# Kernel tuning notes

Measured on AMD Instinct MI355X. Metric: run time of the kernel, lower is better.

## Reference

```python
import jax, jax.numpy as jnp
import numpy as np

DIM = 512
HEADS = 8
RES = 14
HEAD_DIM = DIM // HEADS
N = RES * RES


def _make_bias_idxs(res):
    pts = [(i, j) for i in range(res) for j in range(res)]
    offs = {}
    idxs = []
    for p1 in pts:
        for p2 in pts:
            o = (abs(p1[0] - p2[0]), abs(p1[1] - p2[1]))
            if o not in offs:
                offs[o] = len(offs)
            idxs.append(offs[o])
    return np.asarray(idxs, dtype=np.int32).reshape(res * res, res * res), len(offs)


def setup_inputs() -> dict:
    key = jax.random.key(0)
    ks = jax.random.split(key, 6)
    idxs, n_off = _make_bias_idxs(RES)  # n_off == 196 for res=14
    B = 128
    return {
        "x": jax.random.normal(ks[0], (B, DIM, RES, RES), dtype=jnp.float32),
        "qkv_w": jax.random.normal(ks[1], (3 * DIM, DIM), dtype=jnp.float32) * 0.02,
        "qkv_b": jnp.zeros((3 * DIM,), dtype=jnp.float32),
        "proj_w": jax.random.normal(ks[2], (DIM, DIM), dtype=jnp.float32) * 0.02,
        "proj_b": jnp.zeros((DIM,), dtype=jnp.float32),
        "attention_biases": jax.random.normal(ks[3], (HEADS, n_off), dtype=jnp.float32) * 0.02,
        "bias_idxs": jnp.asarray(idxs),
    }


def reference(x, qkv_w, qkv_b, proj_w, proj_b, attention_biases, bias_idxs):
    B, C, H, W = x.shape
    scale = HEAD_DIM ** -0.5
    # 1x1 conv == channel-wise linear
    qkv = jnp.einsum("oc,bchw->bohw", qkv_w, x) + qkv_b[None, :, None, None]
    q, k, v = jnp.split(qkv, 3, axis=1)
    # [B, heads, head_dim, N]
    q = q.reshape(B, HEADS, HEAD_DIM, N)
    k = k.reshape(B, HEADS, HEAD_DIM, N)
    v = v.reshape(B, HEADS, HEAD_DIM, N)
    attn = jnp.einsum("bhdn,bhdm->bhnm", q, k) * scale  # [B,h,N,N]
    bias = attention_biases[:, bias_idxs]  # gather -> [h,N,N]
    attn = jax.nn.softmax(attn + bias[None], axis=-1)
    out = jnp.einsum("bhnm,bhdm->bhdn", attn, v).reshape(B, C, H, W)
    return jnp.einsum("oc,bchw->bohw", proj_w, out) + proj_b[None, :, None, None]
```

## Files before the change

kernel.cpp:

```cpp
#include <hip/hip_runtime.h>
#include <hip/hip_bf16.h>
#include <math.h>

#define B_     128
#define DIM_   512
#define HEADS_ 8
#define HD_    64
#define N_     196
#define NP_    224
#define NROW_  208
#define SCALE_ 0.125f
#define BSTRIDE (DIM_ * N_)
#define J_     (B_ * NP_)

typedef unsigned short u16;
typedef unsigned int   u32;
typedef __attribute__((ext_vector_type(8))) short bf16x8;
typedef __attribute__((ext_vector_type(4))) float f32x4;

__device__ __forceinline__ u16 f2bf(float f) {
    u32 u = __float_as_uint(f);
    return (u16)((u + 0x7fffu + ((u >> 16) & 1u)) >> 16);
}
__device__ __forceinline__ void gload_lds16(const u16* g, u16* l) {
    __builtin_amdgcn_global_load_lds(
        (const __attribute__((address_space(1))) void*)g,
        (__attribute__((address_space(3))) void*)l, 16, 0, 0);
}

__global__ __launch_bounds__(256) void cvt_bf2(
    const float* __restrict__ a, u16* __restrict__ da, int n4a,
    const float* __restrict__ b, u16* __restrict__ db, int n4b)
{
    const int i = blockIdx.x * 256 + threadIdx.x;
    const float* src = blockIdx.y ? b : a;
    u16* dst = blockIdx.y ? db : da;
    const int n4 = blockIdx.y ? n4b : n4a;
    if (i < n4) {
        const float4 v = reinterpret_cast<const float4*>(src)[i];
        uint2 o;
        o.x = (u32)f2bf(v.x) | ((u32)f2bf(v.y) << 16);
        o.y = (u32)f2bf(v.z) | ((u32)f2bf(v.w) << 16);
        reinterpret_cast<uint2*>(dst)[i] = o;
    }
}

__global__ __launch_bounds__(256) void cvt_xT(
    const float* __restrict__ x, u16* __restrict__ XT)
{
    __shared__ float tile[64][65];
    const int t = threadIdx.x;
    const int jj = t & 63, ii = t >> 6;
    const int ct = blockIdx.x, ntb = blockIdx.y, b = blockIdx.z;
    const float* xb = x + ((size_t)b * DIM_ + ct * 64) * N_;
    const int n0 = ntb * 64;
    #pragma unroll
    for (int s = 0; s < 16; ++s) {
        const int i = ii + s * 4;
        const int n = n0 + jj;
        tile[i][jj] = (n < N_) ? xb[(size_t)i * N_ + n] : 0.f;
    }
    __syncthreads();
    u16* ot = XT + (size_t)b * NP_ * DIM_ + ct * 64;
    #pragma unroll
    for (int s = 0; s < 16; ++s) {
        const int nn = n0 + ii + s * 4;
        if (nn < N_) ot[(size_t)nn * DIM_ + jj] = f2bf(tile[jj][ii + s * 4]);
    }
}

__global__ __launch_bounds__(256) void mk_eb(
    const float* __restrict__ biases, const int* __restrict__ bidx,
    float* __restrict__ EB)
{
    const int n = blockIdx.x, h = blockIdx.y;
    const int m = threadIdx.x;
    if (m < NP_) {
        float v = 0.f;
        if (n < N_ && m < N_) v = __expf(biases[h * N_ + bidx[n * N_ + m]]);
        EB[((size_t)h * NROW_ + n) * NP_ + m] = v;
    }
}

template<bool QKV>
__global__ __launch_bounds__(256) void gemm128(
    const u16* __restrict__ Bt, const u16* __restrict__ W,
    const float* __restrict__ bias,
    u16* __restrict__ o_q, u16* __restrict__ o_k, u16* __restrict__ o_v,
    float* __restrict__ o_f)
{
    __shared__ u16 As[2][128 * 32];
    __shared__ u16 Bs[2][128 * 32];
    const int t = threadIdx.x;
    const int wave = t >> 6, lane = t & 63;
    const int m16 = lane & 15, quad = lane >> 4;

    constexpr int MT  = QKV ? 12 : 4;
    constexpr int NWG = (J_ / 128) * MT;
    const int bid = blockIdx.x;
    const int swz = (bid & 7) * (NWG / 8) + (bid >> 3);
    const int mt = swz % MT;
    const int jt = swz / MT;
    const int m0 = mt * 128, j0 = jt * 128;
    const int wy = wave >> 1, wx = wave & 1;

    const int srow  = (lane >> 2);
    const int schnk = (lane & 3) ^ ((lane >> 3) & 3);
    const u16* gA = W  + (size_t)(m0 + wave * 32 + srow) * DIM_ + schnk * 8;
    const u16* gB = Bt + (size_t)(j0 + wave * 32 + srow) * DIM_ + schnk * 8;

    const int rcol = (quad ^ ((m16 >> 1) & 3)) * 8;

    f32x4 acc[4][4];
    const f32x4 z4 = {0.f, 0.f, 0.f, 0.f};
    #pragma unroll
    for (int fi = 0; fi < 4; ++fi)
        #pragma unroll
        for (int fj = 0; fj < 4; ++fj) acc[fi][fj] = z4;

    #pragma unroll
    for (int cc = 0; cc < 2; ++cc) {
        const int c = wave * 2 + cc;
        gload_lds16(gA + (size_t)(cc * 16) * DIM_, As[0] + c * 512);
        gload_lds16(gB + (size_t)(cc * 16) * DIM_, Bs[0] + c * 512);
    }
    #pragma unroll
    for (int kt = 0; kt < 16; ++kt) {
        const int cur = kt & 1;
        __syncthreads();
        if (kt < 15) {
            #pragma unroll
            for (int cc = 0; cc < 2; ++cc) {
                const int c = wave * 2 + cc;
                gload_lds16(gA + (size_t)(cc * 16) * DIM_ + (kt + 1) * 32, As[cur ^ 1] + c * 512);
                gload_lds16(gB + (size_t)(cc * 16) * DIM_ + (kt + 1) * 32, Bs[cur ^ 1] + c * 512);
            }
        }
        bf16x8 af[4], bf[4];
        #pragma unroll
        for (int fi = 0; fi < 4; ++fi)
            af[fi] = *reinterpret_cast<const bf16x8*>(As[cur] + (wy * 64 + fi * 16 + m16) * 32 + rcol);
        #pragma unroll
        for (int fj = 0; fj < 4; ++fj)
            bf[fj] = *reinterpret_cast<const bf16x8*>(Bs[cur] + (wx * 64 + fj * 16 + m16) * 32 + rcol);
        #pragma unroll
        for (int fi = 0; fi < 4; ++fi)
            #pragma unroll
            for (int fj = 0; fj < 4; ++fj)
                acc[fi][fj] = __builtin_amdgcn_mfma_f32_16x16x32_bf16(af[fi], bf[fj], acc[fi][fj], 0, 0, 0);
    }

    const int mbase = m0 + wy * 64;
    float bb[4][4];
    #pragma unroll
    for (int fi = 0; fi < 4; ++fi)
        #pragma unroll
        for (int r = 0; r < 4; ++r) bb[fi][r] = bias[mbase + fi * 16 + quad * 4 + r];

    if (QKV) {
        const int part = mbase >> 9;
        const int h = (mbase & 511) >> 6;
        #pragma unroll
        for (int fj = 0; fj < 4; ++fj) {
            const int j = j0 + wx * 64 + fj * 16 + m16;
            const u32 b = (u32)j / 224u;
            const int n = j - (int)b * 224;
            if (part < 2) {
                u16* base = (part == 0 ? o_q : o_k) + (((size_t)b * HEADS_ + h) * NP_ + n) * HD_;
                #pragma unroll
                for (int fi = 0; fi < 4; ++fi) {
                    const int d0 = fi * 16 + quad * 4;
                    uint2 pk;
                    pk.x = (u32)f2bf(acc[fi][fj][0] + bb[fi][0]) | ((u32)f2bf(acc[fi][fj][1] + bb[fi][1]) << 16);
                    pk.y = (u32)f2bf(acc[fi][fj][2] + bb[fi][2]) | ((u32)f2bf(acc[fi][fj][3] + bb[fi][3]) << 16);
                    *reinterpret_cast<uint2*>(base + d0) = pk;
                }
            } else {
                u16* vb = o_v + (((size_t)b * HEADS_ + h) * HD_) * NP_ + n;
                #pragma unroll
                for (int fi = 0; fi < 4; ++fi) {
                    const int d0 = fi * 16 + quad * 4;
                    #pragma unroll
                    for (int r = 0; r < 4; ++r)
                        vb[(size_t)(d0 + r) * NP_] = f2bf(acc[fi][fj][r] + bb[fi][r]);
                }
            }
        }
    } else {
        #pragma unroll
        for (int fj = 0; fj < 4; ++fj) {
            const int j = j0 + wx * 64 + fj * 16 + m16;
            const u32 b = (u32)j / 224u;
            const int n = j - (int)b * 224;
            if (n < N_) {
                float* ob = o_f + (size_t)b * BSTRIDE + n;
                #pragma unroll
                for (int fi = 0; fi < 4; ++fi) {
                    const int r0 = mbase + fi * 16 + quad * 4;
                    #pragma unroll
                    for (int r = 0; r < 4; ++r)
                        ob[(size_t)(r0 + r) * N_] = acc[fi][fj][r] + bb[fi][r];
                }
            }
        }
    }
}

__global__ __launch_bounds__(512) void attn_mfma(
    const u16* __restrict__ qT, const u16* __restrict__ kT,
    const u16* __restrict__ vS, const float* __restrict__ EB,
    u16* __restrict__ OT)
{
    __shared__ u16 Ks[224 * 64];
    __shared__ u16 Vs[64 * 232];
    __shared__ u16 P[8][16 * 232];
    const int t = threadIdx.x;
    const int wave = t >> 6, lane = t & 63;
    const int m16 = lane & 15, quad = lane >> 4;
    const int b = blockIdx.x, h = blockIdx.y;
    const u16* qTb = qT + ((size_t)b * HEADS_ + h) * (NP_ * HD_);
    const u16* kTb = kT + ((size_t)b * HEADS_ + h) * (NP_ * HD_);
    const u16* vb  = vS + ((size_t)b * HEADS_ + h) * (HD_ * NP_);
    const float* ebh = EB + (size_t)h * NROW_ * NP_;
    u16* Pw = P[wave];
    u16* otb = OT + (size_t)b * NP_ * DIM_ + h * HD_;
    const f32x4 z4 = {0.f, 0.f, 0.f, 0.f};

    #pragma unroll
    for (int i = 0; i < 4; ++i) {
        const int c = t + i * 512;
        if (c < 1792) {
            const int row = c >> 3, ch = c & 7;
            const bf16x8 d = *reinterpret_cast<const bf16x8*>(kTb + row * HD_ + ch * 8);
            *reinterpret_cast<bf16x8*>(Ks + row * 64 + ((ch ^ (row & 7)) * 8)) = d;
        }
    }
    #pragma unroll
    for (int i = 0; i < 4; ++i) {
        const int c = t + i * 512;
        if (c < 1792) {
            const u32 row = (u32)c / 28u;
            const int ch = c - (int)row * 28;
            const bf16x8 d = *reinterpret_cast<const bf16x8*>(vb + (size_t)row * NP_ + ch * 8);
            *reinterpret_cast<bf16x8*>(Vs + row * 232 + ch * 8) = d;
        }
    }
    __syncthreads();

    for (int nt = wave; nt < 13; nt += 8) {
        f32x4 s[14];
        #pragma unroll
        for (int mt = 0; mt < 14; ++mt) s[mt] = z4;
        #pragma unroll
        for (int ks = 0; ks < 2; ++ks) {
            const bf16x8 a = *reinterpret_cast<const bf16x8*>(
                qTb + (size_t)(nt * 16 + m16) * HD_ + ks * 32 + quad * 8);
            const int ch = ((ks * 4 + quad) ^ (m16 & 7)) * 8;
            #pragma unroll
            for (int mtile = 0; mtile < 14; ++mtile) {
                const bf16x8 bf = *reinterpret_cast<const bf16x8*>(
                    Ks + (mtile * 16 + m16) * 64 + ch);
                s[mtile] = __builtin_amdgcn_mfma_f32_16x16x32_bf16(a, bf, s[mtile], 0, 0, 0);
            }
        }
        float mx[4] = {-INFINITY, -INFINITY, -INFINITY, -INFINITY};
        #pragma unroll
        for (int mt = 0; mt < 14; ++mt)
            #pragma unroll
            for (int r = 0; r < 4; ++r) mx[r] = fmaxf(mx[r], s[mt][r]);
        #pragma unroll
        for (int off = 1; off < 16; off <<= 1)
            #pragma unroll
            for (int r = 0; r < 4; ++r) mx[r] = fmaxf(mx[r], __shfl_xor(mx[r], off, 64));
        #pragma unroll
        for (int r = 0; r < 4; ++r) mx[r] *= SCALE_;

        const float* ebn = ebh + (size_t)(nt * 16 + quad * 4) * NP_ + m16;
        float sum[4] = {0.f, 0.f, 0.f, 0.f};
        #pragma unroll
        for (int mt = 0; mt < 14; ++mt) {
            #pragma unroll
            for (int r = 0; r < 4; ++r) {
                const float e = __expf(fmaf(s[mt][r], SCALE_, -mx[r])) * ebn[(size_t)r * NP_ + mt * 16];
                s[mt][r] = e;
                sum[r] += e;
            }
        }
        #pragma unroll
        for (int off = 1; off < 16; off <<= 1)
            #pragma unroll
            for (int r = 0; r < 4; ++r) sum[r] += __shfl_xor(sum[r], off, 64);
        float inv[4];
        #pragma unroll
        for (int r = 0; r < 4; ++r) inv[r] = 1.f / sum[r];

        #pragma unroll
        for (int mt = 0; mt < 14; ++mt)
            #pragma unroll
            for (int r = 0; r < 4; ++r)
                Pw[(quad * 4 + r) * 232 + mt * 16 + m16] = f2bf(s[mt][r] * inv[r]);

        f32x4 o[4];
        #pragma unroll
        for (int dt = 0; dt < 4; ++dt) o[dt] = z4;
        #pragma unroll
        for (int ks = 0; ks < 7; ++ks) {
            const bf16x8 a = *reinterpret_cast<const bf16x8*>(Pw + m16 * 232 + ks * 32 + quad * 8);
            #pragma unroll
            for (int dt = 0; dt < 4; ++dt) {
                const bf16x8 bf = *reinterpret_cast<const bf16x8*>(
                    Vs + (dt * 16 + m16) * 232 + ks * 32 + quad * 8);
                o[dt] = __builtin_amdgcn_mfma_f32_16x16x32_bf16(a, bf, o[dt], 0, 0, 0);
            }
        }
        #pragma unroll
        for (int r = 0; r < 4; ++r) {
            const int n = nt * 16 + quad * 4 + r;
            if (n < N_) {
                #pragma unroll
                for (int dt = 0; dt < 4; ++dt)
                    otb[(size_t)n * DIM_ + dt * 16 + m16] = f2bf(o[dt][r]);
            }
        }
    }
}

extern "C" void kernel_launch(void* const* d_in, const int* in_sizes, int n_in,
                              void* d_out, int out_size, void* d_ws, size_t ws_size,
                              hipStream_t stream) {
    const float* x      = (const float*)d_in[0];
    const float* qkv_w  = (const float*)d_in[1];
    const float* qkv_b  = (const float*)d_in[2];
    const float* proj_w = (const float*)d_in[3];
    const float* proj_b = (const float*)d_in[4];
    const float* biases = (const float*)d_in[5];
    const int*   bidx   = (const int*)d_in[6];
    float* out = (float*)d_out;

    char* w = (char*)d_ws;
    u16* XT  = (u16*)w; w += (size_t)B_ * NP_ * DIM_ * 2;
    u16* qTw = (u16*)w; w += (size_t)B_ * HEADS_ * NP_ * HD_ * 2;
    u16* vSw = (u16*)w; w += (size_t)B_ * HEADS_ * HD_ * NP_ * 2;
    float* EB = (float*)w; w += (size_t)HEADS_ * NROW_ * NP_ * 4;
    u16* wq  = (u16*)w; w += (size_t)3 * DIM_ * DIM_ * 2;
    u16* wpj = (u16*)w;
    u16* kTw = (u16*)d_out;

    cvt_bf2<<<dim3(768, 2), 256, 0, stream>>>(qkv_w, wq, 3 * DIM_ * DIM_ / 4,
                                              proj_w, wpj, DIM_ * DIM_ / 4);
    cvt_xT<<<dim3(8, 4, B_), 256, 0, stream>>>(x, XT);
    mk_eb<<<dim3(NROW_, HEADS_), 256, 0, stream>>>(biases, bidx, EB);
    gemm128<true><<<dim3((J_ / 128) * 12), 256, 0, stream>>>(XT, wq, qkv_b, qTw, kTw, vSw, nullptr);
    attn_mfma<<<dim3(B_, HEADS_), 512, 0, stream>>>(qTw, kTw, vSw, EB, XT);
    gemm128<false><<<dim3((J_ / 128) * 4), 256, 0, stream>>>(XT, wpj, proj_b, nullptr, nullptr, nullptr, out);
}
```

Measured before the change: 276.5 us.

## Pre-tile GEMM operands into MFMA fragment order and load directly from global

Weights, transposed activations and the attention output are now written in a blocked layout that matches the 16x32 MFMA fragment order, so each lane's bf16x8 operand is one contiguous 16-byte global load. The GEMM drops its LDS double buffer, global_load_lds staging and barriers, and reads A and B fragments straight from global memory. This saves LDS traffic and synchronisation but gives up data reuse through LDS, so each wave re-reads operands through L1/L2. The attention kernel's output stores become scattered 2-byte writes into the tiled layout.

```diff
diff --git a/kernel.cpp b/kernel.cpp
--- a/kernel.cpp
+++ b/kernel.cpp
@@ -22,26 +22,27 @@
     u32 u = __float_as_uint(f);
     return (u16)((u + 0x7fffu + ((u >> 16) & 1u)) >> 16);
 }
-__device__ __forceinline__ void gload_lds16(const u16* g, u16* l) {
-    __builtin_amdgcn_global_load_lds(
-        (const __attribute__((address_space(1))) void*)g,
-        (__attribute__((address_space(3))) void*)l, 16, 0, 0);
-}
-
-__global__ __launch_bounds__(256) void cvt_bf2(
-    const float* __restrict__ a, u16* __restrict__ da, int n4a,
-    const float* __restrict__ b, u16* __restrict__ db, int n4b)
-{
-    const int i = blockIdx.x * 256 + threadIdx.x;
-    const float* src = blockIdx.y ? b : a;
-    u16* dst = blockIdx.y ? db : da;
-    const int n4 = blockIdx.y ? n4b : n4a;
-    if (i < n4) {
-        const float4 v = reinterpret_cast<const float4*>(src)[i];
-        uint2 o;
-        o.x = (u32)f2bf(v.x) | ((u32)f2bf(v.y) << 16);
-        o.y = (u32)f2bf(v.z) | ((u32)f2bf(v.w) << 16);
-        reinterpret_cast<uint2*>(dst)[i] = o;
+
+
+__global__ __launch_bounds__(256) void cvt_w2(
+    const float* __restrict__ qw, u16* __restrict__ qd,
+    const float* __restrict__ pw, u16* __restrict__ pd)
+{
+    const float* src = blockIdx.y ? pw : qw;
+    u16* dst = blockIdx.y ? pd : qd;
+    const int nch = blockIdx.y ? (DIM_ * DIM_ / 8) : (3 * DIM_ * DIM_ / 8);
+    const int t = blockIdx.x * 256 + threadIdx.x;
+    if (t < nch) {
+        const int m16 = t & 15, q = (t >> 4) & 3, kb = (t >> 6) & 15, mb = t >> 10;
+        const float* s = src + (size_t)(mb * 16 + m16) * DIM_ + kb * 32 + q * 8;
+        const float4 v0 = reinterpret_cast<const float4*>(s)[0];
+        const float4 v1 = reinterpret_cast<const float4*>(s)[1];
+        uint4 o;
+        o.x = (u32)f2bf(v0.x) | ((u32)f2bf(v0.y) << 16);
+        o.y = (u32)f2bf(v0.z) | ((u32)f2bf(v0.w) << 16);
+        o.z = (u32)f2bf(v1.x) | ((u32)f2bf(v1.y) << 16);
+        o.w = (u32)f2bf(v1.z) | ((u32)f2bf(v1.w) << 16);
+        reinterpret_cast<uint4*>(dst)[t] = o;
     }
 }
 
@@ -61,11 +62,26 @@
         tile[i][jj] = (n < N_) ? xb[(size_t)i * N_ + n] : 0.f;
     }
     __syncthreads();
-    u16* ot = XT + (size_t)b * NP_ * DIM_ + ct * 64;
-    #pragma unroll
-    for (int s = 0; s < 16; ++s) {
-        const int nn = n0 + ii + s * 4;
-        if (nn < N_) ot[(size_t)nn * DIM_ + jj] = f2bf(tile[jj][ii + s * 4]);
+    const int lo = t & 15, hi = t >> 4;
+    const int c8 = hi & 7, ng = hi >> 3;
+    #pragma unroll
+    for (int s = 0; s < 2; ++s) {
+        const int n_loc = (s * 2 + ng) * 16 + lo;
+        const int nn = n0 + n_loc;
+        if (nn < N_) {
+            const int j = b * NP_ + nn;
+            const int c0 = ct * 64 + c8 * 8;
+            u16 vv[8];
+            #pragma unroll
+            for (int e = 0; e < 8; ++e) vv[e] = f2bf(tile[c8 * 8 + e][n_loc]);
+            uint4 o;
+            o.x = (u32)vv[0] | ((u32)vv[1] << 16);
+            o.y = (u32)vv[2] | ((u32)vv[3] << 16);
+            o.z = (u32)vv[4] | ((u32)vv[5] << 16);
+            o.w = (u32)vv[6] | ((u32)vv[7] << 16);
+            *reinterpret_cast<uint4*>(XT + (size_t)(j >> 4) * 8192
+                + (c0 >> 5) * 512 + ((c0 >> 3) & 3) * 128 + (j & 15) * 8) = o;
+        }
     }
 }
 
@@ -89,8 +105,6 @@
     u16* __restrict__ o_q, u16* __restrict__ o_k, u16* __restrict__ o_v,
     float* __restrict__ o_f)
 {
-    __shared__ u16 As[2][128 * 32];
-    __shared__ u16 Bs[2][128 * 32];
     const int t = threadIdx.x;
     const int wave = t >> 6, lane = t & 63;
     const int m16 = lane & 15, quad = lane >> 4;
@@ -104,12 +118,8 @@
     const int m0 = mt * 128, j0 = jt * 128;
     const int wy = wave >> 1, wx = wave & 1;
 
-    const int srow  = (lane >> 2);
-    const int schnk = (lane & 3) ^ ((lane >> 3) & 3);
-    const u16* gA = W  + (size_t)(m0 + wave * 32 + srow) * DIM_ + schnk * 8;
-    const u16* gB = Bt + (size_t)(j0 + wave * 32 + srow) * DIM_ + schnk * 8;
-
-    const int rcol = (quad ^ ((m16 >> 1) & 3)) * 8;
+    const u16* A2 = W  + (size_t)(mt * 8 + wy * 4) * 8192 + quad * 128 + m16 * 8;
+    const u16* B2 = Bt + (size_t)(jt * 8 + wx * 4) * 8192 + quad * 128 + m16 * 8;
 
     f32x4 acc[4][4];
     const f32x4 z4 = {0.f, 0.f, 0.f, 0.f};
@@ -119,30 +129,14 @@
         for (int fj = 0; fj < 4; ++fj) acc[fi][fj] = z4;
 
     #pragma unroll
-    for (int cc = 0; cc < 2; ++cc) {
-        const int c = wave * 2 + cc;
-        gload_lds16(gA + (size_t)(cc * 16) * DIM_, As[0] + c * 512);
-        gload_lds16(gB + (size_t)(cc * 16) * DIM_, Bs[0] + c * 512);
-    }
-    #pragma unroll
     for (int kt = 0; kt < 16; ++kt) {
-        const int cur = kt & 1;
-        __syncthreads();
-        if (kt < 15) {
-            #pragma unroll
-            for (int cc = 0; cc < 2; ++cc) {
-                const int c = wave * 2 + cc;
-                gload_lds16(gA + (size_t)(cc * 16) * DIM_ + (kt + 1) * 32, As[cur ^ 1] + c * 512);
-                gload_lds16(gB + (size_t)(cc * 16) * DIM_ + (kt + 1) * 32, Bs[cur ^ 1] + c * 512);
-            }
-        }
         bf16x8 af[4], bf[4];
         #pragma unroll
         for (int fi = 0; fi < 4; ++fi)
-            af[fi] = *reinterpret_cast<const bf16x8*>(As[cur] + (wy * 64 + fi * 16 + m16) * 32 + rcol);
+            af[fi] = *reinterpret_cast<const bf16x8*>(A2 + fi * 8192 + kt * 512);
         #pragma unroll
         for (int fj = 0; fj < 4; ++fj)
-            bf[fj] = *reinterpret_cast<const bf16x8*>(Bs[cur] + (wx * 64 + fj * 16 + m16) * 32 + rcol);
+            bf[fj] = *reinterpret_cast<const bf16x8*>(B2 + fj * 8192 + kt * 512);
         #pragma unroll
         for (int fi = 0; fi < 4; ++fi)
             #pragma unroll
@@ -223,7 +217,6 @@
     const u16* vb  = vS + ((size_t)b * HEADS_ + h) * (HD_ * NP_);
     const float* ebh = EB + (size_t)h * NROW_ * NP_;
     u16* Pw = P[wave];
-    u16* otb = OT + (size_t)b * NP_ * DIM_ + h * HD_;
     const f32x4 z4 = {0.f, 0.f, 0.f, 0.f};
 
     #pragma unroll
@@ -317,9 +310,13 @@
         for (int r = 0; r < 4; ++r) {
             const int n = nt * 16 + quad * 4 + r;
             if (n < N_) {
+                const int j = b * NP_ + n;
                 #pragma unroll
-                for (int dt = 0; dt < 4; ++dt)
-                    otb[(size_t)n * DIM_ + dt * 16 + m16] = f2bf(o[dt][r]);
+                for (int dt = 0; dt < 4; ++dt) {
+                    const int c = h * HD_ + dt * 16 + m16;
+                    OT[(size_t)(j >> 4) * 8192 + (c >> 5) * 512
+                       + ((c >> 3) & 3) * 128 + (j & 15) * 8 + (c & 7)] = f2bf(o[dt][r]);
+                }
             }
         }
     }
@@ -346,8 +343,7 @@
     u16* wpj = (u16*)w;
     u16* kTw = (u16*)d_out;
 
-    cvt_bf2<<<dim3(768, 2), 256, 0, stream>>>(qkv_w, wq, 3 * DIM_ * DIM_ / 4,
-                                              proj_w, wpj, DIM_ * DIM_ / 4);
+    cvt_w2<<<dim3(384, 2), 256, 0, stream>>>(qkv_w, wq, proj_w, wpj);
     cvt_xT<<<dim3(8, 4, B_), 256, 0, stream>>>(x, XT);
     mk_eb<<<dim3(NROW_, HEADS_), 256, 0, stream>>>(biases, bidx, EB);
     gemm128<true><<<dim3((J_ / 128) * 12), 256, 0, stream>>>(XT, wq, qkv_b, qTw, kTw, vSw, nullptr);
```

Result: slower. 292.2 us (+5.7%).
